# Kernel optimization log

Measured on AMD Instinct MI355X. Metric: run time of the kernel, lower is better.

The kernel has to match this reference:

```python
import jax, jax.numpy as jnp
import numpy as np

ALPHA = 0.7
NUM_HEADS = 12
NUM_KV_HEADS = 6
HEAD_DIM = 64
ROPE_BASE = 10000.0


def ternary_quantize(w):
    thr = ALPHA * jnp.mean(jnp.abs(w))
    return jnp.sign(w) * (jnp.abs(w) >= thr).astype(w.dtype)


def bitlinear(x, w):
    # forward: F.linear(x, ternary(w)) * mean(|w|)
    scale = jnp.mean(jnp.abs(w))
    qw = ternary_quantize(w)
    return (x @ qw.T) * scale


def rope_tables(seq_len, dim, dtype):
    inv_freq = 1.0 / (ROPE_BASE ** (jnp.arange(0, dim, 2, dtype=jnp.float32) / dim))
    t = jnp.arange(seq_len, dtype=jnp.float32)
    freqs = jnp.outer(t, inv_freq)            # [S, dim/2]
    emb = jnp.concatenate([freqs, freqs], -1)  # [S, dim]
    return jnp.cos(emb).astype(dtype), jnp.sin(emb).astype(dtype)


def rotate_half(x):
    x1, x2 = jnp.split(x, 2, axis=-1)
    return jnp.concatenate([-x2, x1], axis=-1)


def setup_inputs() -> dict:
    key = jax.random.key(0)
    ks = jax.random.split(key, 5)
    B, S, H = 2, 2048, 768
    return {
        "hidden_states": jax.random.normal(ks[0], (B, S, H), jnp.float32),
        "Wq": jax.random.normal(ks[1], (768, 768), jnp.float32) * 0.02,
        "Wk": jax.random.normal(ks[2], (384, 768), jnp.float32) * 0.02,
        "Wv": jax.random.normal(ks[3], (384, 768), jnp.float32) * 0.02,
        "Wo": jax.random.normal(ks[4], (768, 768), jnp.float32) * 0.02,
    }


def reference(hidden_states, Wq, Wk, Wv, Wo):
    B, S, H = hidden_states.shape
    nh, nkv, hd = NUM_HEADS, NUM_KV_HEADS, HEAD_DIM
    groups = nh // nkv

    q = bitlinear(hidden_states, Wq).reshape(B, S, nh, hd).transpose(0, 2, 1, 3)
    k = bitlinear(hidden_states, Wk).reshape(B, S, nkv, hd).transpose(0, 2, 1, 3)
    v = bitlinear(hidden_states, Wv).reshape(B, S, nkv, hd).transpose(0, 2, 1, 3)

    cos, sin = rope_tables(S, hd, hidden_states.dtype)  # [S, hd]
    cos = cos[None, None]  # [1,1,S,hd]
    sin = sin[None, None]
    q = q * cos + rotate_half(q) * sin
    k = k * cos + rotate_half(k) * sin

    # GQA: expand kv heads to full head count
    k = jnp.repeat(k, groups, axis=1)  # [B, nh, S, hd]
    v = jnp.repeat(v, groups, axis=1)

    scale = 1.0 / jnp.sqrt(jnp.asarray(hd, hidden_states.dtype))
    scores = jnp.einsum("bhsd,bhtd->bhst", q, k) * scale
    attn = jax.nn.softmax(scores, axis=-1)
    out = jnp.einsum("bhst,bhtd->bhsd", attn, v)
    out = out.transpose(0, 2, 1, 3).reshape(B, S, H)
    return bitlinear(out, Wo)
```

## Files before the change

### kernel.cpp

```cpp
#include <hip/hip_runtime.h>
#include <cmath>

typedef unsigned short u16;
typedef unsigned int u32;
typedef __bf16 bf16x2 __attribute__((ext_vector_type(2)));
typedef __bf16 bf16x8 __attribute__((ext_vector_type(8)));
typedef float f32x16 __attribute__((ext_vector_type(16)));

#define NQ (768*768)
#define NK (384*768)

__device__ __forceinline__ u16 f2bf(float f) {
  u32 u = __float_as_uint(f);
  u32 r = (u + 0x7FFFu + ((u >> 16) & 1u)) >> 16;
  return (u16)r;
}
__device__ __forceinline__ u32 packbf(float a, float b) {
#if __has_builtin(__builtin_amdgcn_cvt_pk_bf16_f32)
  bf16x2 v = __builtin_amdgcn_cvt_pk_bf16_f32(a, b);
  u32 r; __builtin_memcpy(&r, &v, 4); return r;
#else
  return (u32)f2bf(a) | ((u32)f2bf(b) << 16);
#endif
}
__device__ __forceinline__ float fexp2(float x) {
#if __has_builtin(__builtin_amdgcn_exp2f)
  return __builtin_amdgcn_exp2f(x);
#else
  return exp2f(x);
#endif
}
__device__ __forceinline__ bf16x8 ldfrag(const u16* p) { bf16x8 v; __builtin_memcpy(&v, p, 16); return v; }
__device__ __forceinline__ f32x16 mfma32_(bf16x8 a, bf16x8 b, f32x16 c) {
  return __builtin_amdgcn_mfma_f32_32x32x16_bf16(a, b, c, 0, 0, 0);
}

__device__ __forceinline__ int kidx(int b6kvh, int s, int d) {
  return b6kvh * 131072 + (s >> 5) * 2048 + (d >> 4) * 512 +
         ((s & 31) + 32 * ((d >> 3) & 1)) * 8 + (d & 7);
}
__device__ __forceinline__ int qidx(int b, int s, int h, int d) {
  return ((b * 64 + (s >> 5)) * 12 + h) * 2048 + (d >> 4) * 512 +
         ((s & 31) + 32 * ((d >> 3) & 1)) * 8 + (d & 7);
}
__device__ __forceinline__ int vidx(int b6kvh, int d, int p) {
  return b6kvh * 131072 + (p >> 6) * 4096 + (d >> 5) * 2048 + ((p >> 4) & 3) * 512 +
         ((d & 31) + 32 * ((p >> 3) & 1)) * 8 + (p & 7);
}
__device__ __forceinline__ int fidx(int m, int k) {
  return (m >> 5) * 24576 + (k >> 4) * 512 + ((m & 31) + 32 * ((k >> 3) & 1)) * 8 + (k & 7);
}

__global__ __launch_bounds__(256) void abssum_kernel(const float* __restrict__ wq, const float* __restrict__ wk,
                                                     const float* __restrict__ wv, const float* __restrict__ wo,
                                                     float* __restrict__ sums) {
  int which = blockIdx.y;
  const float* w = (which == 0) ? wq : (which == 1) ? wk : (which == 2) ? wv : wo;
  int n4 = ((which == 0 || which == 3) ? NQ : NK) >> 2;
  const float4* w4 = (const float4*)w;
  float s = 0.f;
  for (int i = blockIdx.x * blockDim.x + threadIdx.x; i < n4; i += gridDim.x * blockDim.x) {
    float4 v = w4[i];
    s += fabsf(v.x) + fabsf(v.y) + fabsf(v.z) + fabsf(v.w);
  }
  for (int off = 32; off; off >>= 1) s += __shfl_down(s, off);
  __shared__ float ls[4];
  if ((threadIdx.x & 63) == 0) ls[threadIdx.x >> 6] = s;
  __syncthreads();
  if (threadIdx.x == 0) atomicAdd(&sums[which], ls[0] + ls[1] + ls[2] + ls[3]);
}

__global__ __launch_bounds__(256) void quant_kernel(const float* __restrict__ wq, const float* __restrict__ wk,
                                                    const float* __restrict__ wv, const float* __restrict__ wo,
                                                    const float* __restrict__ sums,
                                                    u16* __restrict__ qw, u16* __restrict__ woq) {
  float thr0 = 0.7f * sums[0] * (1.f / NQ);
  float thr1 = 0.7f * sums[1] * (1.f / NK);
  float thr2 = 0.7f * sums[2] * (1.f / NK);
  float thr3 = 0.7f * sums[3] * (1.f / NQ);
  const int NQKV = NQ + 2 * NK;
  const int total = NQKV + NQ;
  for (int i = blockIdx.x * blockDim.x + threadIdx.x; i < total; i += gridDim.x * blockDim.x) {
    float v, th; u16* dst;
    if (i < NQ)            { v = wq[i];            th = thr0; dst = &qw[i]; }
    else if (i < NQ + NK)  { v = wk[i - NQ];       th = thr1; dst = &qw[i]; }
    else if (i < NQKV)     { v = wv[i - NQ - NK];  th = thr2; dst = &qw[i]; }
    else                   { v = wo[i - NQKV];     th = thr3; dst = &woq[i - NQKV]; }
    float q = (fabsf(v) >= th) ? ((v > 0.f) ? 1.f : -1.f) : 0.f;
    *dst = f2bf(q);
  }
}

__global__ __launch_bounds__(256) void castx_kernel(const float* __restrict__ x, u16* __restrict__ xb) {
  int idx = blockIdx.x * blockDim.x + threadIdx.x;
  int m = idx / 96, k8 = idx - m * 96;
  const float4* xp = (const float4*)(x + m * 768 + k8 * 8);
  float4 v0 = xp[0], v1 = xp[1];
  u16 o[8] = { f2bf(v0.x), f2bf(v0.y), f2bf(v0.z), f2bf(v0.w),
               f2bf(v1.x), f2bf(v1.y), f2bf(v1.z), f2bf(v1.w) };
  u16* dst = xb + (m >> 5) * 24576 + (k8 >> 1) * 512 + ((m & 31) + 32 * (k8 & 1)) * 8;
  __builtin_memcpy(dst, o, 16);
}

__device__ __forceinline__ void gemm_tile_64x128(const u16* __restrict__ A, const u16* __restrict__ Bw,
                                                 u16* Bt, int tm, int tn, f32x16 acc[2]) {
  int t = threadIdx.x, lane = t & 63, w = t >> 6, c = lane & 31, g2 = lane >> 5;
  int wm = w & 1, wn = w >> 1;
  const u16* abase = A + (tm * 2 + wm) * 24576 + lane * 8;
  for (int k0 = 0; k0 < 768; k0 += 64) {
#pragma unroll
    for (int rd = 0; rd < 4; rd++) {
      int ch = (rd * 4 + w) * 64 + lane;
      int n = ch >> 3, jp = ch & 7;
      int jl = jp ^ (n & 7);
      const u16* gp = Bw + (tn * 128 + n) * 768 + k0 + jl * 8;
      __builtin_amdgcn_global_load_lds((const __attribute__((address_space(1))) u32*)gp,
                                       (__attribute__((address_space(3))) u32*)(Bt + (rd * 4 + w) * 512),
                                       16, 0, 0);
    }
    bf16x8 af[4];
#pragma unroll
    for (int ks = 0; ks < 4; ks++) af[ks] = ldfrag(abase + ((k0 >> 4) + ks) * 512);
    __syncthreads();
#pragma unroll
    for (int ks = 0; ks < 4; ks++) {
#pragma unroll
      for (int nb = 0; nb < 2; nb++) {
        int n = wn * 64 + nb * 32 + c;
        int jp = (ks * 2 + g2) ^ (n & 7);
        bf16x8 bf = ldfrag(Bt + n * 64 + jp * 8);
        acc[nb] = mfma32_(af[ks], bf, acc[nb]);
      }
    }
    __syncthreads();
  }
}

__global__ __launch_bounds__(256, 4) void gemm_qkv_kernel(const u16* __restrict__ xb, const u16* __restrict__ qw,
                                                          const float* __restrict__ sums,
                                                          u16* __restrict__ qb, u16* __restrict__ kb,
                                                          u16* __restrict__ vT) {
  __shared__ u16 Bt[8192];
  int tn = blockIdx.x, tm = blockIdx.y;
  f32x16 acc[2]; acc[0] = (f32x16)0.f; acc[1] = (f32x16)0.f;
  gemm_tile_64x128(xb, qw, Bt, tm, tn, acc);
  int t = threadIdx.x, lane = t & 63, w = t >> 6, c = lane & 31, g2 = lane >> 5;
  int wm = w & 1, wn = w >> 1;
  float sq = sums[0] * (1.f / NQ) * 0.180336880111120f;
  float sk = sums[1] * (1.f / NK);
  float sv = sums[2] * (1.f / NK);
  int mb = tm * 64 + wm * 32 + 4 * g2;
  if (tn < 9) {
    float sc = (tn < 6) ? sq : sk;
    int head = (tn < 6) ? (tn * 2 + wn) : ((tn - 6) * 2 + wn);
    float f = fexp2((float)c * -0.41524101186092029f);
#pragma unroll
    for (int r = 0; r < 16; r++) {
      int m = mb + (r & 3) + 8 * (r >> 2);
      int bb = m >> 11, s = m & 2047;
      float sn, cs; sincosf((float)s * f, &sn, &cs);
      float x1 = acc[0][r] * sc, x2 = acc[1][r] * sc;
      u16 y1 = f2bf(x1 * cs - x2 * sn);
      u16 y2 = f2bf(x2 * cs + x1 * sn);
      if (tn < 6) {
        qb[qidx(bb, s, head, c)]      = y1;
        qb[qidx(bb, s, head, c + 32)] = y2;
      } else {
        kb[kidx(bb * 6 + head, s, c)]      = y1;
        kb[kidx(bb * 6 + head, s, c + 32)] = y2;
      }
    }
  } else {
    int kvh = (tn - 9) * 2 + wn;
#pragma unroll
    for (int nb = 0; nb < 2; nb++)
#pragma unroll
      for (int r = 0; r < 16; r++) {
        int m = mb + (r & 3) + 8 * (r >> 2);
        int bb = m >> 11, s = m & 2047;
        int sp = (s & ~12) | ((s & 4) << 1) | ((s & 8) >> 1);
        vT[vidx(bb * 6 + kvh, nb * 32 + c, sp)] = f2bf(acc[nb][r] * sv);
      }
  }
}

__global__ __launch_bounds__(256, 3) void attn_kernel(const u16* __restrict__ qb, const u16* __restrict__ kb,
                                                      const u16* __restrict__ vT, u16* __restrict__ ab) {
  __shared__ float Obuf[4][32][66];
  __shared__ float Lbuf[4][32];
  int qt = blockIdx.x, bk = blockIdx.y;
  int b = bk / 6, kvh = bk % 6;
  int t = threadIdx.x, lane = t & 63, w = t >> 6, c = lane & 31, g2 = lane >> 5;
  int qn = w & 1, kh = w >> 1;

  const u16* qbase = qb + ((b * 64 + qt) * 12 + kvh * 2 + qn) * 2048;
  bf16x8 qf[4];
#pragma unroll
  for (int ks = 0; ks < 4; ks++) qf[ks] = ldfrag(qbase + ks * 512 + lane * 8);

  u32 onesw = 0x3F803F80u;
  bf16x8 ones;
  { u32 tmp[4] = {onesw, onesw, onesw, onesw}; __builtin_memcpy(&ones, tmp, 16); }

  f32x16 fz = (f32x16)0.f;
  f32x16 O[2] = {fz, fz};
  f32x16 Lacc = fz;

  const u16* Kb = kb + bk * 131072;
  const u16* Vb = vT + bk * 131072;

  for (int it = 0; it < 32; it++) {
    int kb32 = kh * 32 + it;
    const u16* kt = Kb + kb32 * 2048;
    const u16* vt = Vb + (kb32 >> 1) * 4096 + (kb32 & 1) * 1024;
    bf16x8 kf[4];
#pragma unroll
    for (int ks = 0; ks < 4; ks++) kf[ks] = ldfrag(kt + ks * 512 + lane * 8);
    bf16x8 vf[2][2];
#pragma unroll
    for (int dn = 0; dn < 2; dn++)
#pragma unroll
      for (int ksv = 0; ksv < 2; ksv++)
        vf[dn][ksv] = ldfrag(vt + dn * 2048 + ksv * 512 + lane * 8);
    f32x16 S = fz;
#pragma unroll
    for (int ks = 0; ks < 4; ks++) S = mfma32_(kf[ks], qf[ks], S);
    float e[16];
#pragma unroll
    for (int r = 0; r < 16; r++) e[r] = fexp2(S[r]);
    u32 P[8];
#pragma unroll
    for (int j = 0; j < 8; j++) P[j] = packbf(e[2 * j], e[2 * j + 1]);
    bf16x8 PA[2];
    __builtin_memcpy(&PA[0], &P[0], 16);
    __builtin_memcpy(&PA[1], &P[4], 16);
#pragma unroll
    for (int ksv = 0; ksv < 2; ksv++) {
      O[0] = mfma32_(PA[ksv], vf[0][ksv], O[0]);
      O[1] = mfma32_(PA[ksv], vf[1][ksv], O[1]);
      Lacc = mfma32_(PA[ksv], ones, Lacc);
    }
  }
  if (c == 0) {
#pragma unroll
    for (int r = 0; r < 16; r++) Lbuf[w][(r & 3) + 8 * (r >> 2) + 4 * g2] = Lacc[r];
  }
#pragma unroll
  for (int dn = 0; dn < 2; dn++)
#pragma unroll
    for (int r = 0; r < 16; r++)
      Obuf[w][(r & 3) + 8 * (r >> 2) + 4 * g2][dn * 32 + c] = O[dn][r];
  __syncthreads();
  {
    int hn = t >> 7, qq = (t >> 2) & 31, dc = (t & 3) * 16;
    float l = Lbuf[hn][qq] + Lbuf[hn + 2][qq];
    float inv = 1.f / l;
    u16 o[16];
#pragma unroll
    for (int j = 0; j < 16; j++)
      o[j] = f2bf((Obuf[hn][qq][dc + j] + Obuf[hn + 2][qq][dc + j]) * inv);
    int h = kvh * 2 + hn;
    int mg = b * 64 + qt;
    u16* dst = ab + mg * 24576 + ((h * 64 + dc) >> 4) * 512 + qq * 8;
    __builtin_memcpy(dst, o, 16);
    __builtin_memcpy(dst + 256, o + 8, 16);
  }
}

__global__ __launch_bounds__(256, 4) void gemm_out_kernel(const u16* __restrict__ ab, const u16* __restrict__ woq,
                                                          const float* __restrict__ sums, float* __restrict__ out) {
  __shared__ u16 Bt[4096];
  int tn = blockIdx.x, tm = blockIdx.y;
  int t = threadIdx.x, lane = t & 63, w = t >> 6, c = lane & 31, g2 = lane >> 5;
  int wm = w & 1, wn = w >> 1;
  f32x16 acc = (f32x16)0.f;
  const u16* abase = ab + (tm * 2 + wm) * 24576 + lane * 8;
  for (int k0 = 0; k0 < 768; k0 += 64) {
#pragma unroll
    for (int rd = 0; rd < 2; rd++) {
      int ch = (rd * 4 + w) * 64 + lane;
      int n = ch >> 3, jp = ch & 7;
      int jl = jp ^ (n & 7);
      const u16* gp = woq + (tn * 64 + n) * 768 + k0 + jl * 8;
      __builtin_amdgcn_global_load_lds((const __attribute__((address_space(1))) u32*)gp,
                                       (__attribute__((address_space(3))) u32*)(Bt + (rd * 4 + w) * 512),
                                       16, 0, 0);
    }
    bf16x8 af[4];
#pragma unroll
    for (int ks = 0; ks < 4; ks++) af[ks] = ldfrag(abase + ((k0 >> 4) + ks) * 512);
    __syncthreads();
#pragma unroll
    for (int ks = 0; ks < 4; ks++) {
      int n = wn * 32 + c;
      int jp = (ks * 2 + g2) ^ (n & 7);
      bf16x8 bf = ldfrag(Bt + n * 64 + jp * 8);
      acc = mfma32_(af[ks], bf, acc);
    }
    __syncthreads();
  }
  float so = sums[3] * (1.f / NQ);
  int mb = tm * 64 + wm * 32 + 4 * g2;
#pragma unroll
  for (int r = 0; r < 16; r++) {
    int m = mb + (r & 3) + 8 * (r >> 2);
    out[m * 768 + tn * 64 + wn * 32 + c] = acc[r] * so;
  }
}

extern "C" void kernel_launch(void* const* d_in, const int* in_sizes, int n_in,
                              void* d_out, int out_size, void* d_ws, size_t ws_size,
                              hipStream_t stream) {
  const float* x  = (const float*)d_in[0];
  const float* wq = (const float*)d_in[1];
  const float* wk = (const float*)d_in[2];
  const float* wv = (const float*)d_in[3];
  const float* wo = (const float*)d_in[4];
  float* out = (float*)d_out;
  char* ws = (char*)d_ws;

  float* sums = (float*)ws;
  u16* qw  = (u16*)(ws + 256);
  u16* woq = (u16*)(ws + 2359552);
  u16* xb  = (u16*)(ws + 3539200);
  u16* qb  = (u16*)(ws + 9830656);
  u16* kb  = (u16*)(ws + 16122112);
  u16* vT  = (u16*)(ws + 19267840);
  u16* ab  = (u16*)(ws + 22413568);

  hipMemsetAsync(sums, 0, 16, stream);
  dim3 blk(256);
  abssum_kernel<<<dim3(64, 4), blk, 0, stream>>>(wq, wk, wv, wo, sums);
  quant_kernel<<<dim3(6912), blk, 0, stream>>>(wq, wk, wv, wo, sums, qw, woq);
  castx_kernel<<<dim3(1536), blk, 0, stream>>>(x, xb);
  gemm_qkv_kernel<<<dim3(12, 64), blk, 0, stream>>>(xb, qw, sums, qb, kb, vT);
  attn_kernel<<<dim3(64, 12), blk, 0, stream>>>(qb, kb, vT, ab);
  gemm_out_kernel<<<dim3(12, 64), blk, 0, stream>>>(ab, woq, sums, out);
}
```

Before: 157.5 us.

## Prepack weights into MFMA fragment layout and drop LDS staging in GEMMs

The quantize and cast kernels are merged into one prep kernel. It writes the ternary weights directly in the MFMA fragment layout, so both GEMMs can load B fragments straight from global memory without LDS staging or __syncthreads. The attention grid is transposed so consecutive blocks share a kv head, which may improve K/V cache reuse. The cost is more direct global loads per wave with no LDS sharing of B across waves, and lower launch-bounds occupancy hints.

```diff
diff --git a/kernel.cpp b/kernel.cpp
--- a/kernel.cpp
+++ b/kernel.cpp
@@ -35,6 +35,9 @@
   return __builtin_amdgcn_mfma_f32_32x32x16_bf16(a, b, c, 0, 0, 0);
 }
 
+__device__ __forceinline__ int fidx(int r, int k) {
+  return (r >> 5) * 24576 + (k >> 4) * 512 + ((r & 31) + 32 * ((k >> 3) & 1)) * 8 + (k & 7);
+}
 __device__ __forceinline__ int kidx(int b6kvh, int s, int d) {
   return b6kvh * 131072 + (s >> 5) * 2048 + (d >> 4) * 512 +
          ((s & 31) + 32 * ((d >> 3) & 1)) * 8 + (d & 7);
@@ -46,9 +49,6 @@
 __device__ __forceinline__ int vidx(int b6kvh, int d, int p) {
   return b6kvh * 131072 + (p >> 6) * 4096 + (d >> 5) * 2048 + ((p >> 4) & 3) * 512 +
          ((d & 31) + 32 * ((p >> 3) & 1)) * 8 + (p & 7);
-}
-__device__ __forceinline__ int fidx(int m, int k) {
-  return (m >> 5) * 24576 + (k >> 4) * 512 + ((m & 31) + 32 * ((k >> 3) & 1)) * 8 + (k & 7);
 }
 
 __global__ __launch_bounds__(256) void abssum_kernel(const float* __restrict__ wq, const float* __restrict__ wk,
@@ -70,82 +70,59 @@
   if (threadIdx.x == 0) atomicAdd(&sums[which], ls[0] + ls[1] + ls[2] + ls[3]);
 }
 
-__global__ __launch_bounds__(256) void quant_kernel(const float* __restrict__ wq, const float* __restrict__ wk,
-                                                    const float* __restrict__ wv, const float* __restrict__ wo,
-                                                    const float* __restrict__ sums,
-                                                    u16* __restrict__ qw, u16* __restrict__ woq) {
-  float thr0 = 0.7f * sums[0] * (1.f / NQ);
-  float thr1 = 0.7f * sums[1] * (1.f / NK);
-  float thr2 = 0.7f * sums[2] * (1.f / NK);
-  float thr3 = 0.7f * sums[3] * (1.f / NQ);
-  const int NQKV = NQ + 2 * NK;
-  const int total = NQKV + NQ;
-  for (int i = blockIdx.x * blockDim.x + threadIdx.x; i < total; i += gridDim.x * blockDim.x) {
-    float v, th; u16* dst;
-    if (i < NQ)            { v = wq[i];            th = thr0; dst = &qw[i]; }
-    else if (i < NQ + NK)  { v = wk[i - NQ];       th = thr1; dst = &qw[i]; }
-    else if (i < NQKV)     { v = wv[i - NQ - NK];  th = thr2; dst = &qw[i]; }
-    else                   { v = wo[i - NQKV];     th = thr3; dst = &woq[i - NQKV]; }
-    float q = (fabsf(v) >= th) ? ((v > 0.f) ? 1.f : -1.f) : 0.f;
-    *dst = f2bf(q);
-  }
-}
-
-__global__ __launch_bounds__(256) void castx_kernel(const float* __restrict__ x, u16* __restrict__ xb) {
-  int idx = blockIdx.x * blockDim.x + threadIdx.x;
-  int m = idx / 96, k8 = idx - m * 96;
-  const float4* xp = (const float4*)(x + m * 768 + k8 * 8);
-  float4 v0 = xp[0], v1 = xp[1];
-  u16 o[8] = { f2bf(v0.x), f2bf(v0.y), f2bf(v0.z), f2bf(v0.w),
-               f2bf(v1.x), f2bf(v1.y), f2bf(v1.z), f2bf(v1.w) };
-  u16* dst = xb + (m >> 5) * 24576 + (k8 >> 1) * 512 + ((m & 31) + 32 * (k8 & 1)) * 8;
-  __builtin_memcpy(dst, o, 16);
-}
-
-__device__ __forceinline__ void gemm_tile_64x128(const u16* __restrict__ A, const u16* __restrict__ Bw,
-                                                 u16* Bt, int tm, int tn, f32x16 acc[2]) {
-  int t = threadIdx.x, lane = t & 63, w = t >> 6, c = lane & 31, g2 = lane >> 5;
-  int wm = w & 1, wn = w >> 1;
-  const u16* abase = A + (tm * 2 + wm) * 24576 + lane * 8;
-  for (int k0 = 0; k0 < 768; k0 += 64) {
-#pragma unroll
-    for (int rd = 0; rd < 4; rd++) {
-      int ch = (rd * 4 + w) * 64 + lane;
-      int n = ch >> 3, jp = ch & 7;
-      int jl = jp ^ (n & 7);
-      const u16* gp = Bw + (tn * 128 + n) * 768 + k0 + jl * 8;
-      __builtin_amdgcn_global_load_lds((const __attribute__((address_space(1))) u32*)gp,
-                                       (__attribute__((address_space(3))) u32*)(Bt + (rd * 4 + w) * 512),
-                                       16, 0, 0);
-    }
-    bf16x8 af[4];
-#pragma unroll
-    for (int ks = 0; ks < 4; ks++) af[ks] = ldfrag(abase + ((k0 >> 4) + ks) * 512);
-    __syncthreads();
-#pragma unroll
-    for (int ks = 0; ks < 4; ks++) {
-#pragma unroll
-      for (int nb = 0; nb < 2; nb++) {
-        int n = wn * 64 + nb * 32 + c;
-        int jp = (ks * 2 + g2) ^ (n & 7);
-        bf16x8 bf = ldfrag(Bt + n * 64 + jp * 8);
-        acc[nb] = mfma32_(af[ks], bf, acc[nb]);
-      }
-    }
-    __syncthreads();
-  }
-}
-
-__global__ __launch_bounds__(256, 4) void gemm_qkv_kernel(const u16* __restrict__ xb, const u16* __restrict__ qw,
+__global__ __launch_bounds__(256) void prep_kernel(const float* __restrict__ wq, const float* __restrict__ wk,
+                                                   const float* __restrict__ wv, const float* __restrict__ wo,
+                                                   const float* __restrict__ sums, const float* __restrict__ x,
+                                                   u16* __restrict__ qw, u16* __restrict__ woq,
+                                                   u16* __restrict__ xb) {
+  int i = blockIdx.x * blockDim.x + threadIdx.x;
+  if (i < 221184) {
+    int n = i / 96, k8 = i - n * 96;
+    const float* src; float th; u16* dst; int nd;
+    if (n < 768)       { src = wq + n * 768;          th = 0.7f * sums[0] * (1.f / NQ); dst = qw;  nd = n; }
+    else if (n < 1152) { src = wk + (n - 768) * 768;  th = 0.7f * sums[1] * (1.f / NK); dst = qw;  nd = n; }
+    else if (n < 1536) { src = wv + (n - 1152) * 768; th = 0.7f * sums[2] * (1.f / NK); dst = qw;  nd = n; }
+    else               { src = wo + (n - 1536) * 768; th = 0.7f * sums[3] * (1.f / NQ); dst = woq; nd = n - 1536; }
+    const float4* sp = (const float4*)(src + k8 * 8);
+    float4 v0 = sp[0], v1 = sp[1];
+    float e[8] = {v0.x, v0.y, v0.z, v0.w, v1.x, v1.y, v1.z, v1.w};
+    u16 o[8];
+#pragma unroll
+    for (int j = 0; j < 8; j++)
+      o[j] = f2bf((fabsf(e[j]) >= th) ? ((e[j] > 0.f) ? 1.f : -1.f) : 0.f);
+    __builtin_memcpy(dst + fidx(nd, k8 * 8), o, 16);
+  } else {
+    int j = i - 221184;
+    int m = j / 96, k8 = j - m * 96;
+    const float4* xp = (const float4*)(x + m * 768 + k8 * 8);
+    float4 v0 = xp[0], v1 = xp[1];
+    u16 o[8] = { f2bf(v0.x), f2bf(v0.y), f2bf(v0.z), f2bf(v0.w),
+                 f2bf(v1.x), f2bf(v1.y), f2bf(v1.z), f2bf(v1.w) };
+    __builtin_memcpy(xb + fidx(m, k8 * 8), o, 16);
+  }
+}
+
+__global__ __launch_bounds__(256, 3) void gemm_qkv_kernel(const u16* __restrict__ xb, const u16* __restrict__ qw,
                                                           const float* __restrict__ sums,
                                                           u16* __restrict__ qb, u16* __restrict__ kb,
                                                           u16* __restrict__ vT) {
-  __shared__ u16 Bt[8192];
   int tn = blockIdx.x, tm = blockIdx.y;
-  f32x16 acc[2]; acc[0] = (f32x16)0.f; acc[1] = (f32x16)0.f;
-  gemm_tile_64x128(xb, qw, Bt, tm, tn, acc);
   int t = threadIdx.x, lane = t & 63, w = t >> 6, c = lane & 31, g2 = lane >> 5;
   int wm = w & 1, wn = w >> 1;
+  const u16* abase = xb + (tm * 2 + wm) * 24576 + lane * 8;
+  const u16* bbase0 = qw + (tn * 4 + wn * 2) * 24576 + lane * 8;
+  const u16* bbase1 = bbase0 + 24576;
+  f32x16 acc[2]; acc[0] = (f32x16)0.f; acc[1] = (f32x16)0.f;
+  for (int kk = 0; kk < 48; kk += 4) {
+#pragma unroll
+    for (int ks = 0; ks < 4; ks++) {
+      bf16x8 af = ldfrag(abase + (kk + ks) * 512);
+      bf16x8 b0 = ldfrag(bbase0 + (kk + ks) * 512);
+      bf16x8 b1 = ldfrag(bbase1 + (kk + ks) * 512);
+      acc[0] = mfma32_(af, b0, acc[0]);
+      acc[1] = mfma32_(af, b1, acc[1]);
+    }
+  }
   float sq = sums[0] * (1.f / NQ) * 0.180336880111120f;
   float sk = sums[1] * (1.f / NK);
   float sv = sums[2] * (1.f / NK);
@@ -188,7 +165,7 @@
                                                       const u16* __restrict__ vT, u16* __restrict__ ab) {
   __shared__ float Obuf[4][32][66];
   __shared__ float Lbuf[4][32];
-  int qt = blockIdx.x, bk = blockIdx.y;
+  int bk = blockIdx.x, qt = blockIdx.y;
   int b = bk / 6, kvh = bk % 6;
   int t = threadIdx.x, lane = t & 63, w = t >> 6, c = lane & 31, g2 = lane >> 5;
   int qn = w & 1, kh = w >> 1;
@@ -267,37 +244,21 @@
   }
 }
 
-__global__ __launch_bounds__(256, 4) void gemm_out_kernel(const u16* __restrict__ ab, const u16* __restrict__ woq,
+__global__ __launch_bounds__(256, 3) void gemm_out_kernel(const u16* __restrict__ ab, const u16* __restrict__ woq,
                                                           const float* __restrict__ sums, float* __restrict__ out) {
-  __shared__ u16 Bt[4096];
   int tn = blockIdx.x, tm = blockIdx.y;
   int t = threadIdx.x, lane = t & 63, w = t >> 6, c = lane & 31, g2 = lane >> 5;
   int wm = w & 1, wn = w >> 1;
+  const u16* abase = ab + (tm * 2 + wm) * 24576 + lane * 8;
+  const u16* bbase = woq + (tn * 2 + wn) * 24576 + lane * 8;
   f32x16 acc = (f32x16)0.f;
-  const u16* abase = ab + (tm * 2 + wm) * 24576 + lane * 8;
-  for (int k0 = 0; k0 < 768; k0 += 64) {
-#pragma unroll
-    for (int rd = 0; rd < 2; rd++) {
-      int ch = (rd * 4 + w) * 64 + lane;
-      int n = ch >> 3, jp = ch & 7;
-      int jl = jp ^ (n & 7);
-      const u16* gp = woq + (tn * 64 + n) * 768 + k0 + jl * 8;
-      __builtin_amdgcn_global_load_lds((const __attribute__((address_space(1))) u32*)gp,
-                                       (__attribute__((address_space(3))) u32*)(Bt + (rd * 4 + w) * 512),
-                                       16, 0, 0);
-    }
-    bf16x8 af[4];
-#pragma unroll
-    for (int ks = 0; ks < 4; ks++) af[ks] = ldfrag(abase + ((k0 >> 4) + ks) * 512);
-    __syncthreads();
+  for (int kk = 0; kk < 48; kk += 4) {
 #pragma unroll
     for (int ks = 0; ks < 4; ks++) {
-      int n = wn * 32 + c;
-      int jp = (ks * 2 + g2) ^ (n & 7);
-      bf16x8 bf = ldfrag(Bt + n * 64 + jp * 8);
-      acc = mfma32_(af[ks], bf, acc);
-    }
-    __syncthreads();
+      bf16x8 af = ldfrag(abase + (kk + ks) * 512);
+      bf16x8 bf = ldfrag(bbase + (kk + ks) * 512);
+      acc = mfma32_(af, bf, acc);
+    }
   }
   float so = sums[3] * (1.f / NQ);
   int mb = tm * 64 + wm * 32 + 4 * g2;
@@ -331,9 +292,8 @@
   hipMemsetAsync(sums, 0, 16, stream);
   dim3 blk(256);
   abssum_kernel<<<dim3(64, 4), blk, 0, stream>>>(wq, wk, wv, wo, sums);
-  quant_kernel<<<dim3(6912), blk, 0, stream>>>(wq, wk, wv, wo, sums, qw, woq);
-  castx_kernel<<<dim3(1536), blk, 0, stream>>>(x, xb);
+  prep_kernel<<<dim3(2400), blk, 0, stream>>>(wq, wk, wv, wo, sums, x, qw, woq, xb);
   gemm_qkv_kernel<<<dim3(12, 64), blk, 0, stream>>>(xb, qw, sums, qb, kb, vT);
-  attn_kernel<<<dim3(64, 12), blk, 0, stream>>>(qb, kb, vT, ab);
+  attn_kernel<<<dim3(12, 64), blk, 0, stream>>>(qb, kb, vT, ab);
   gemm_out_kernel<<<dim3(12, 64), blk, 0, stream>>>(ab, woq, sums, out);
 }
```

Result: no change. 156.9 us (-0.4%).
